# Performance work log

Measured on AMD Instinct MI355X. Metric: run time of the kernel, lower is better.

## Reference

```python
import jax, jax.numpy as jnp
import numpy as np

EPS_ENT = 1e-08


def setup_inputs() -> dict:
    key = jax.random.key(0)
    k1, k2, k3, k4 = jax.random.split(key, 4)
    B, K, D = 128, 64, 256      # batch, slots, d_model
    BD, NC = 2700, 1024          # basis_dim, num_codes
    slot_features = jax.random.normal(k1, (B, K, D), dtype=jnp.float32)
    W_proj = jax.random.normal(k2, (BD, D), dtype=jnp.float32) * (1.0 / np.sqrt(D))
    b_proj = jax.random.normal(k3, (BD,), dtype=jnp.float32) * 0.01
    embed = jax.random.normal(k4, (NC, BD), dtype=jnp.float32)
    return {"slot_features": slot_features, "W_proj": W_proj, "b_proj": b_proj, "embed": embed}


def reference(slot_features, W_proj, b_proj, embed):
    b, k, _ = slot_features.shape
    num_codes, basis_dim = embed.shape
    # slot_proj: Linear(d_model -> basis_dim)
    z_e = jnp.einsum('bkd,ed->bke', slot_features, W_proj) + b_proj  # [B,K,BD]
    z_flat = z_e.reshape(b * k, basis_dim)
    # squared-euclidean distances: ||z||^2 - 2 z e^T + ||e||^2  -> [B*K, NC]
    dist = (jnp.sum(z_flat * z_flat, axis=1, keepdims=True)
            - 2.0 * (z_flat @ embed.T)
            + jnp.sum(embed * embed, axis=1)[None, :])
    indices_flat = jnp.argmin(dist, axis=-1)                # [B*K]
    indices = indices_flat.reshape(b, k)
    e_i = embed[indices_flat].reshape(b, k, basis_dim)      # gather codebook atoms
    # straight-through estimator
    q_st = z_e + jax.lax.stop_gradient(e_i - z_e)
    vq_loss = jnp.mean((z_e - jax.lax.stop_gradient(e_i)) ** 2)
    # entropy diversity bonus over soft assignment distribution
    probs = jax.nn.softmax(-dist, axis=-1)                  # [B*K, NC]
    avg_probs = jnp.mean(probs, axis=0)
    entropy = -jnp.sum(avg_probs * jnp.log(avg_probs + EPS_ENT))
    return (q_st, indices, vq_loss, entropy)
```

## Files before the change

kernel.cpp:

```cpp
#include <hip/hip_runtime.h>
#include <stdint.h>
#include <stddef.h>

static constexpr int    M_ROWS = 8192;
static constexpr int    DMODEL = 256;
static constexpr int    BDIM   = 2700;
static constexpr int    NCODES = 1024;
static constexpr int    KP     = 2720;
static constexpr int    NPAD   = 2816;
static constexpr size_t QST_N  = (size_t)M_ROWS * (size_t)BDIM;
static constexpr int    MAX_CAND = 32768;

typedef __bf16 bf16x8 __attribute__((ext_vector_type(8)));
typedef float  f32x4  __attribute__((ext_vector_type(4)));

__device__ inline unsigned short bf16h(float x) {
    unsigned u = __float_as_uint(x);
    unsigned r = u + 0x7fffu + ((u >> 16) & 1u);
    return (unsigned short)(r >> 16);
}
__device__ inline float bf2f(unsigned short h) {
    return __uint_as_float(((unsigned)h) << 16);
}
__device__ inline void split3(float x, unsigned short& h, unsigned short& m,
                              unsigned short& l) {
    h = bf16h(x);
    const float r1 = x - bf2f(h);
    m = bf16h(r1);
    l = bf16h(r1 - bf2f(m));
}
__device__ inline unsigned long long pack_key(float v, int idx) {
    unsigned u = __float_as_uint(v);
    unsigned k = (u & 0x80000000u) ? ~u : (u | 0x80000000u);
    return ((unsigned long long)k << 32) | (unsigned)idx;
}
__device__ inline float unpack_val(unsigned long long key) {
    unsigned ku = (unsigned)(key >> 32);
    return (ku & 0x80000000u) ? __uint_as_float(ku & 0x7fffffffu)
                              : __uint_as_float(~ku);
}

__global__ __launch_bounds__(256)
void eprep(const float* __restrict__ emb, unsigned short* __restrict__ eh,
           float* __restrict__ esq, float* __restrict__ prob,
           float* __restrict__ sse, int* __restrict__ ccount,
           float* __restrict__ zsq)
{
    const int row = blockIdx.x;
    const int tid = threadIdx.x;
    if (tid < 8) zsq[row * 8 + tid] = 0.0f;
    if (tid == 0) prob[row] = 0.0f;
    if (row == 0 && tid == 0) { sse[0] = 0.0f; ccount[0] = 0; }

    float acc = 0.0f;
    for (int g = tid; g < KP / 4; g += 256) {
        const int c = g * 4;
        ushort4 h;
        if (c < BDIM) {
            const float4 v = *reinterpret_cast<const float4*>(emb + (size_t)row * BDIM + c);
            h.x = bf16h(v.x); h.y = bf16h(v.y); h.z = bf16h(v.z); h.w = bf16h(v.w);
            acc += v.x * v.x + v.y * v.y + v.z * v.z + v.w * v.w;
        } else {
            h.x = h.y = h.z = h.w = 0;
        }
        *reinterpret_cast<ushort4*>(eh + (size_t)row * KP + c) = h;
    }
    for (int off = 32; off; off >>= 1) acc += __shfl_down(acc, off);
    __shared__ float wsum[4];
    if ((tid & 63) == 0) wsum[tid >> 6] = acc;
    __syncthreads();
    if (tid == 0) esq[row] = wsum[0] + wsum[1] + wsum[2] + wsum[3];
}

__global__ __launch_bounds__(256)
void ssplit3(const float* __restrict__ slot, unsigned short* __restrict__ sh,
             unsigned short* __restrict__ sm, unsigned short* __restrict__ sl)
{
    const size_t i = (size_t)blockIdx.x * 256 + threadIdx.x;
    const float4 v = reinterpret_cast<const float4*>(slot)[i];
    ushort4 h, m, l;
    split3(v.x, h.x, m.x, l.x); split3(v.y, h.y, m.y, l.y);
    split3(v.z, h.z, m.z, l.z); split3(v.w, h.w, m.w, l.w);
    reinterpret_cast<ushort4*>(sh)[i] = h;
    reinterpret_cast<ushort4*>(sm)[i] = m;
    reinterpret_cast<ushort4*>(sl)[i] = l;
}

__global__ __launch_bounds__(64)
void wsplit3(const float* __restrict__ W, unsigned short* __restrict__ wh,
             unsigned short* __restrict__ wm, unsigned short* __restrict__ wl)
{
    const int row = blockIdx.x;
    const int c   = threadIdx.x * 4;
    ushort4 h, m, l;
    if (row < BDIM) {
        const float4 v = *reinterpret_cast<const float4*>(W + (size_t)row * DMODEL + c);
        split3(v.x, h.x, m.x, l.x); split3(v.y, h.y, m.y, l.y);
        split3(v.z, h.z, m.z, l.z); split3(v.w, h.w, m.w, l.w);
    } else {
        h.x = h.y = h.z = h.w = 0; m = h; l = h;
    }
    const size_t off = (size_t)row * DMODEL + c;
    *reinterpret_cast<ushort4*>(wh + off) = h;
    *reinterpret_cast<ushort4*>(wm + off) = m;
    *reinterpret_cast<ushort4*>(wl + off) = l;
}

__global__ __launch_bounds__(256, 2)
void gemm1_mfma(const unsigned short* __restrict__ Ah_, const unsigned short* __restrict__ Am_,
                const unsigned short* __restrict__ Al_,
                const unsigned short* __restrict__ Bh_, const unsigned short* __restrict__ Bm_,
                const unsigned short* __restrict__ Bl_,
                const float* __restrict__ bias, float* __restrict__ Z,
                unsigned short* __restrict__ zh, float* __restrict__ zsq)
{
    constexpr int NT = DMODEL / 32;
    __shared__ unsigned short lds[2][3 * 4096 + 3 * 2048];

    const int tid  = threadIdx.x;
    const int wid  = tid >> 6;
    const int lane = tid & 63;
    const int bid  = blockIdx.x;
    const int xcd  = bid & 7;
    const int q    = bid >> 3;
    const int row0 = (xcd * 8 + q / 44) << 7;
    const int col0 = (q % 44) << 6;
    const int wr = wid >> 1, wc = wid & 1;

    f32x4 acc[4][2];
#pragma unroll
    for (int m = 0; m < 4; ++m)
#pragma unroll
        for (int n = 0; n < 2; ++n) acc[m][n] = (f32x4)0.0f;

    auto stage = [&](int t, int b) {
        const int kt = t * 32;
#pragma unroll
        for (int T = 0; T < 3; ++T) {
            const unsigned short* src = (T == 0) ? Ah_ : (T == 1) ? Am_ : Al_;
#pragma unroll
            for (int qq = 0; qq < 2; ++qq) {
                const int chunk = wid * 2 + qq;
                const int r     = chunk * 16 + (lane >> 2);
                const int unswz = ((lane & 3) << 4) ^ ((r & 3) << 4);
                const unsigned short* g = src + (size_t)(row0 + r) * DMODEL + kt + (unswz >> 1);
                __builtin_amdgcn_global_load_lds(
                    (const __attribute__((address_space(1))) void*)g,
                    (__attribute__((address_space(3))) void*)(&lds[b][T * 4096 + chunk * 512]),
                    16, 0, 0);
            }
        }
#pragma unroll
        for (int T = 0; T < 3; ++T) {
            const unsigned short* src = (T == 0) ? Bh_ : (T == 1) ? Bm_ : Bl_;
            const int chunk = wid;
            const int r     = chunk * 16 + (lane >> 2);
            const int unswz = ((lane & 3) << 4) ^ ((r & 3) << 4);
            const unsigned short* g = src + (size_t)(col0 + r) * DMODEL + kt + (unswz >> 1);
            __builtin_amdgcn_global_load_lds(
                (const __attribute__((address_space(1))) void*)g,
                (__attribute__((address_space(3))) void*)(&lds[b][12288 + T * 2048 + chunk * 512]),
                16, 0, 0);
        }
    };

    auto compute = [&](int b) {
        bf16x8 ah[4], am[4], al[4], bh[2], bm[2], bl[2];
        const int kb = (lane >> 4) << 4;
#pragma unroll
        for (int m = 0; m < 4; ++m) {
            const int r   = wr * 64 + m * 16 + (lane & 15);
            const int off = r * 32 + ((kb ^ ((r & 3) << 4)) >> 1);
            ah[m] = *reinterpret_cast<const bf16x8*>(&lds[b][off]);
            am[m] = *reinterpret_cast<const bf16x8*>(&lds[b][4096 + off]);
            al[m] = *reinterpret_cast<const bf16x8*>(&lds[b][8192 + off]);
        }
#pragma unroll
        for (int n = 0; n < 2; ++n) {
            const int r   = wc * 32 + n * 16 + (lane & 15);
            const int off = r * 32 + ((kb ^ ((r & 3) << 4)) >> 1);
            bh[n] = *reinterpret_cast<const bf16x8*>(&lds[b][12288 + off]);
            bm[n] = *reinterpret_cast<const bf16x8*>(&lds[b][14336 + off]);
            bl[n] = *reinterpret_cast<const bf16x8*>(&lds[b][16384 + off]);
        }
#pragma unroll
        for (int m = 0; m < 4; ++m)
#pragma unroll
            for (int n = 0; n < 2; ++n) {
                acc[m][n] = __builtin_amdgcn_mfma_f32_16x16x32_bf16(ah[m], bh[n], acc[m][n], 0, 0, 0);
                acc[m][n] = __builtin_amdgcn_mfma_f32_16x16x32_bf16(ah[m], bm[n], acc[m][n], 0, 0, 0);
                acc[m][n] = __builtin_amdgcn_mfma_f32_16x16x32_bf16(am[m], bh[n], acc[m][n], 0, 0, 0);
                acc[m][n] = __builtin_amdgcn_mfma_f32_16x16x32_bf16(ah[m], bl[n], acc[m][n], 0, 0, 0);
                acc[m][n] = __builtin_amdgcn_mfma_f32_16x16x32_bf16(am[m], bm[n], acc[m][n], 0, 0, 0);
                acc[m][n] = __builtin_amdgcn_mfma_f32_16x16x32_bf16(al[m], bh[n], acc[m][n], 0, 0, 0);
            }
    };

    stage(0, 0);
    __syncthreads();
    for (int t = 0; t < NT; ++t) {
        const int cur = t & 1;
        if (t + 1 < NT) stage(t + 1, cur ^ 1);
        compute(cur);
        __syncthreads();
    }

    float bv[2];
    int   cv[2];
#pragma unroll
    for (int n = 0; n < 2; ++n) {
        cv[n] = col0 + wc * 32 + n * 16 + (lane & 15);
        bv[n] = (cv[n] < BDIM) ? bias[cv[n]] : 0.0f;
    }
#pragma unroll
    for (int m = 0; m < 4; ++m) {
        const int gr0 = row0 + wr * 64 + m * 16 + ((lane >> 4) << 2);
#pragma unroll
        for (int r = 0; r < 4; ++r) {
            const int gr = gr0 + r;
            float s2 = 0.0f;
#pragma unroll
            for (int n = 0; n < 2; ++n) {
                if (cv[n] < BDIM) {
                    const float z = acc[m][n][r] + bv[n];
                    Z[(size_t)gr * BDIM + cv[n]] = z;
                    zh[(size_t)gr * KP + cv[n]] = bf16h(z);
                    s2 = __builtin_fmaf(z, z, s2);
                } else if (cv[n] < KP) {
                    zh[(size_t)gr * KP + cv[n]] = 0;
                }
            }
            s2 += __shfl_xor(s2, 1);
            s2 += __shfl_xor(s2, 2);
            s2 += __shfl_xor(s2, 4);
            s2 += __shfl_xor(s2, 8);
            if ((lane & 15) == 0) atomicAdd(&zsq[gr], s2);
        }
    }
}

__global__ __launch_bounds__(256, 2)
void gemm2_mfma(const unsigned short* __restrict__ Ah, const unsigned short* __restrict__ Bh,
                const float* __restrict__ zsq, const float* __restrict__ esq,
                float* __restrict__ dist)
{
    constexpr int NT = KP / 32;
    __shared__ unsigned short lds[2][2][128 * 32];

    const int tid  = threadIdx.x;
    const int wid  = tid >> 6;
    const int lane = tid & 63;
    const int bid  = blockIdx.x;
    const int row0 = (bid >> 3) << 7;
    const int col0 = (bid & 7) << 7;
    const int wr = wid >> 1, wc = wid & 1;

    f32x4 acc[4][4];
#pragma unroll
    for (int m = 0; m < 4; ++m)
#pragma unroll
        for (int n = 0; n < 4; ++n) acc[m][n] = (f32x4)0.0f;

    auto stage = [&](int t, int b) {
        const int kt = t * 32;
#pragma unroll
        for (int T = 0; T < 2; ++T) {
            const int base = T ? col0 : row0;
            const unsigned short* src = T ? Bh : Ah;
#pragma unroll
            for (int q = 0; q < 2; ++q) {
                const int chunk = wid * 2 + q;
                const int r     = chunk * 16 + (lane >> 2);
                const int unswz = ((lane & 3) << 4) ^ ((r & 3) << 4);
                const unsigned short* g = src + (size_t)(base + r) * KP + kt + (unswz >> 1);
                __builtin_amdgcn_global_load_lds(
                    (const __attribute__((address_space(1))) void*)g,
                    (__attribute__((address_space(3))) void*)(&lds[b][T][chunk * 512]),
                    16, 0, 0);
            }
        }
    };

    auto compute = [&](int b) {
        bf16x8 ah[4], bh[4];
        const int kb = (lane >> 4) << 4;
#pragma unroll
        for (int m = 0; m < 4; ++m) {
            const int r   = wr * 64 + m * 16 + (lane & 15);
            const int off = r * 32 + ((kb ^ ((r & 3) << 4)) >> 1);
            ah[m] = *reinterpret_cast<const bf16x8*>(&lds[b][0][off]);
        }
#pragma unroll
        for (int n = 0; n < 4; ++n) {
            const int r   = wc * 64 + n * 16 + (lane & 15);
            const int off = r * 32 + ((kb ^ ((r & 3) << 4)) >> 1);
            bh[n] = *reinterpret_cast<const bf16x8*>(&lds[b][1][off]);
        }
#pragma unroll
        for (int m = 0; m < 4; ++m)
#pragma unroll
            for (int n = 0; n < 4; ++n)
                acc[m][n] = __builtin_amdgcn_mfma_f32_16x16x32_bf16(ah[m], bh[n], acc[m][n], 0, 0, 0);
    };

    stage(0, 0);
    __syncthreads();
    for (int t = 0; t < NT; ++t) {
        const int cur = t & 1;
        if (t + 1 < NT) stage(t + 1, cur ^ 1);
        compute(cur);
        __syncthreads();
    }

#pragma unroll
    for (int m = 0; m < 4; ++m) {
        const int gr0 = row0 + wr * 64 + m * 16 + ((lane >> 4) << 2);
#pragma unroll
        for (int n = 0; n < 4; ++n) {
            const int gc = col0 + wc * 64 + n * 16 + (lane & 15);
            const float eq = esq[gc];
#pragma unroll
            for (int r = 0; r < 4; ++r) {
                const int gr = gr0 + r;
                dist[(size_t)gr * NCODES + gc] = zsq[gr] - 2.0f * acc[m][n][r] + eq;
            }
        }
    }
}

static constexpr float DELTA = 3.0f;

__global__ __launch_bounds__(256)
void row_softmax32(const float* __restrict__ dist, float* __restrict__ prob_acc,
                   float* __restrict__ sse, float* __restrict__ out_idx_f,
                   int* __restrict__ out_idx_i, float* __restrict__ gap_out,
                   unsigned* __restrict__ cand, int* __restrict__ cand_count,
                   unsigned long long* __restrict__ row_best)
{
    const int tid = threadIdx.x;
    __shared__ unsigned long long wm0[4], wm1[4];
    __shared__ float wred[4];
    float pacc[4] = {0.f, 0.f, 0.f, 0.f};
    float sse_loc = 0.f;

    for (int rr = 0; rr < 32; ++rr) {
        const int row = blockIdx.x * 32 + rr;
        const float4 d4 = reinterpret_cast<const float4*>(dist + (size_t)row * NCODES)[tid];
        const float dv[4] = {d4.x, d4.y, d4.z, d4.w};

        unsigned long long b0 = 0xFFFFFFFFFFFFFFFFull, b1 = 0xFFFFFFFFFFFFFFFFull;
#pragma unroll
        for (int j = 0; j < 4; ++j) {
            const unsigned long long k = pack_key(dv[j], tid * 4 + j);
            if (k < b0) { b1 = b0; b0 = k; } else if (k < b1) { b1 = k; }
        }
        for (int off = 1; off < 64; off <<= 1) {
            const unsigned long long o0 = __shfl_xor(b0, off);
            const unsigned long long o1 = __shfl_xor(b1, off);
            const unsigned long long nb0 = (b0 < o0) ? b0 : o0;
            const unsigned long long mx  = (b0 < o0) ? o0 : b0;
            const unsigned long long mn1 = (b1 < o1) ? b1 : o1;
            b0 = nb0;
            b1 = (mx < mn1) ? mx : mn1;
        }
        __syncthreads();
        if ((tid & 63) == 0) { wm0[tid >> 6] = b0; wm1[tid >> 6] = b1; }
        __syncthreads();
        unsigned long long B0 = wm0[0], B1 = wm1[0];
#pragma unroll
        for (int w = 1; w < 4; ++w) {
            const unsigned long long o0 = wm0[w], o1 = wm1[w];
            const unsigned long long nb0 = (B0 < o0) ? B0 : o0;
            const unsigned long long mx  = (B0 < o0) ? o0 : B0;
            const unsigned long long mn1 = (B1 < o1) ? B1 : o1;
            B0 = nb0;
            B1 = (mx < mn1) ? mx : mn1;
        }
        const float m   = unpack_val(B0);
        const int   idx = (int)(B0 & 0xffffffffu);
        const float gap = unpack_val(B1) - m;

        if (gap < DELTA) {
            if (tid == 0) row_best[row] = 0xFFFFFFFFFFFFFFFFull;
#pragma unroll
            for (int j = 0; j < 4; ++j) {
                if (dv[j] - m < DELTA) {
                    const int slot = atomicAdd(cand_count, 1);
                    if (slot < MAX_CAND)
                        cand[slot] = ((unsigned)row << 10) | (unsigned)(tid * 4 + j);
                }
            }
        }

        float e[4];
        float s_local = 0.0f;
#pragma unroll
        for (int j = 0; j < 4; ++j) { e[j] = expf(m - dv[j]); s_local += e[j]; }
        for (int off = 32; off; off >>= 1) s_local += __shfl_down(s_local, off);
        if ((tid & 63) == 0) wred[tid >> 6] = s_local;
        __syncthreads();
        const float S = wred[0] + wred[1] + wred[2] + wred[3];
        const float inv = 1.0f / S;
#pragma unroll
        for (int j = 0; j < 4; ++j) pacc[j] += e[j] * inv;

        if (tid == 0) {
            out_idx_f[row] = (float)idx;
            out_idx_i[row] = idx;
            gap_out[row]   = gap;
            sse_loc += m;
        }
    }

    const float scale = 0.0001220703125f;
#pragma unroll
    for (int j = 0; j < 4; ++j)
        if (pacc[j] > 0.0f) atomicAdd(&prob_acc[tid * 4 + j], pacc[j] * scale);
    if (tid == 0) atomicAdd(sse, sse_loc);
}

__global__ __launch_bounds__(256)
void refine2(const float* __restrict__ Zf, const float* __restrict__ emb,
             const unsigned* __restrict__ cand, const int* __restrict__ cand_count,
             const float* __restrict__ zsq, const float* __restrict__ esq,
             unsigned long long* __restrict__ row_best)
{
    const int nwaves = gridDim.x * 4;
    const int wglob  = blockIdx.x * 4 + (threadIdx.x >> 6);
    const int lane   = threadIdx.x & 63;
    const int n = min(*cand_count, MAX_CAND);
    for (int e = wglob; e < n; e += nwaves) {
        const unsigned pc  = cand[e];
        const int row  = (int)(pc >> 10);
        const int code = (int)(pc & 1023u);
        const float4* zp = reinterpret_cast<const float4*>(Zf + (size_t)row * BDIM);
        const float4* ep = reinterpret_cast<const float4*>(emb + (size_t)code * BDIM);
        float a0 = 0, a1 = 0, a2 = 0, a3 = 0;
        for (int k = lane; k < BDIM / 4; k += 64) {
            const float4 z4 = zp[k];
            const float4 e4 = ep[k];
            a0 = __builtin_fmaf(z4.x, e4.x, a0);
            a1 = __builtin_fmaf(z4.y, e4.y, a1);
            a2 = __builtin_fmaf(z4.z, e4.z, a2);
            a3 = __builtin_fmaf(z4.w, e4.w, a3);
        }
        float t = (a0 + a1) + (a2 + a3);
        for (int off = 32; off; off >>= 1) t += __shfl_down(t, off);
        if (lane == 0) {
            const float d = zsq[row] - 2.0f * t + esq[code];
            atomicMin(&row_best[row], pack_key(d, code));
        }
    }
}

__global__ __launch_bounds__(256)
void gather_fix(const float* __restrict__ embed, const float* __restrict__ gap,
                const unsigned long long* __restrict__ row_best,
                int* __restrict__ idxi, float* __restrict__ idxf,
                float* __restrict__ q)
{
    const int row = blockIdx.x;
    __shared__ int code_s;
    if (threadIdx.x == 0) {
        int code = idxi[row];
        if (gap[row] < DELTA) {
            const unsigned long long k = row_best[row];
            if (k != 0xFFFFFFFFFFFFFFFFull) {
                code = (int)(k & 0xffffffffu);
                idxi[row] = code;
                idxf[row] = (float)code;
            }
        }
        code_s = code;
    }
    __syncthreads();
    const int code = code_s;
    const float4* s = reinterpret_cast<const float4*>(embed + (size_t)code * BDIM);
    float4*       d = reinterpret_cast<float4*>(q + (size_t)row * BDIM);
    for (int i = threadIdx.x; i < (BDIM >> 2); i += 256) d[i] = s[i];
}

__global__ __launch_bounds__(256)
void finalize(const float* __restrict__ prob_acc, const float* __restrict__ sse,
              float* __restrict__ out)
{
    const int tid = threadIdx.x;
    float ent = 0.0f;
    for (int c = tid; c < NCODES; c += 256) {
        const float a = prob_acc[c];
        ent -= a * logf(a + 1e-8f);
    }
    for (int off = 32; off; off >>= 1) ent += __shfl_down(ent, off);
    __shared__ float wred[4];
    if ((tid & 63) == 0) wred[tid >> 6] = ent;
    __syncthreads();
    if (tid == 0) {
        out[QST_N + M_ROWS + 0] = sse[0] / 22118400.0f;
        out[QST_N + M_ROWS + 1] = wred[0] + wred[1] + wred[2] + wred[3];
    }
}

extern "C" void kernel_launch(void* const* d_in, const int* in_sizes, int n_in,
                              void* d_out, int out_size, void* d_ws, size_t ws_size,
                              hipStream_t stream)
{
    (void)in_sizes; (void)n_in; (void)out_size; (void)ws_size;
    const float* slot = (const float*)d_in[0];
    const float* W    = (const float*)d_in[1];
    const float* bpr  = (const float*)d_in[2];
    const float* emb  = (const float*)d_in[3];

    float* out  = (float*)d_out;
    float* Z    = out;
    float* idxf = out + QST_N;

    const size_t DIST_B = (size_t)M_ROWS * NCODES * 4;
    const size_t ZH_B   = (size_t)M_ROWS * KP * 2;
    const size_t EH_B   = (size_t)NCODES * KP * 2;

    char* w = (char*)d_ws;
    float* dist = (float*)w;                          w += DIST_B;
    const size_t SSPL_B = (size_t)M_ROWS * DMODEL * 2;
    const size_t WSPL_B = (size_t)NPAD   * DMODEL * 2;
    unsigned short* sh3 = (unsigned short*)(char*)dist;
    unsigned short* sm3 = (unsigned short*)((char*)dist + SSPL_B);
    unsigned short* sl3 = (unsigned short*)((char*)dist + 2 * SSPL_B);
    unsigned short* wh3 = (unsigned short*)((char*)dist + 3 * SSPL_B);
    unsigned short* wm3 = (unsigned short*)((char*)dist + 3 * SSPL_B + WSPL_B);
    unsigned short* wl3 = (unsigned short*)((char*)dist + 3 * SSPL_B + 2 * WSPL_B);

    unsigned short* zh = (unsigned short*)w;          w += ZH_B;
    unsigned short* eh = (unsigned short*)w;          w += EH_B;
    float* zsq  = (float*)w;                          w += (size_t)M_ROWS * 4;
    float* esq  = (float*)w;                          w += (size_t)NCODES * 4;
    float* gap  = (float*)w;                          w += (size_t)M_ROWS * 4;
    int*   idxi = (int*)w;                            w += (size_t)M_ROWS * 4;
    float* prob = (float*)w;                          w += (size_t)NCODES * 4;
    float* sse  = (float*)w;                          w += 256;
    unsigned long long* rbest = (unsigned long long*)w; w += (size_t)M_ROWS * 8;
    unsigned* cand = (unsigned*)w;                    w += (size_t)MAX_CAND * 4;
    int* ccount = (int*)w;

    eprep<<<NCODES, 256, 0, stream>>>(emb, eh, esq, prob, sse, ccount, zsq);
    ssplit3<<<(M_ROWS * DMODEL / 4) / 256, 256, 0, stream>>>(slot, sh3, sm3, sl3);
    wsplit3<<<NPAD, 64, 0, stream>>>(W, wh3, wm3, wl3);
    gemm1_mfma<<<(NPAD / 64) * (M_ROWS / 128), 256, 0, stream>>>(
        sh3, sm3, sl3, wh3, wm3, wl3, bpr, Z, zh, zsq);
    gemm2_mfma<<<(NCODES / 128) * (M_ROWS / 128), 256, 0, stream>>>(
        zh, eh, zsq, esq, dist);
    row_softmax32<<<M_ROWS / 32, 256, 0, stream>>>(dist, prob, sse, idxf, idxi, gap,
                                                   cand, ccount, rbest);
    refine2<<<256, 256, 0, stream>>>(Z, emb, cand, ccount, zsq, esq, rbest);
    gather_fix<<<M_ROWS, 256, 0, stream>>>(emb, gap, rbest, idxi, idxf, Z);
    finalize<<<1, 256, 0, stream>>>(prob, sse, out);
}
```

Before: 409.0 us.

## Use bf16x2 split for projection GEMM and merge prep kernels

```diff
diff --git a/kernel.cpp b/kernel.cpp
--- a/kernel.cpp
+++ b/kernel.cpp
@@ -22,12 +22,9 @@
 __device__ inline float bf2f(unsigned short h) {
     return __uint_as_float(((unsigned)h) << 16);
 }
-__device__ inline void split3(float x, unsigned short& h, unsigned short& m,
-                              unsigned short& l) {
+__device__ inline void split2(float x, unsigned short& h, unsigned short& l) {
     h = bf16h(x);
-    const float r1 = x - bf2f(h);
-    m = bf16h(r1);
-    l = bf16h(r1 - bf2f(m));
+    l = bf16h(x - bf2f(h));
 }
 __device__ inline unsigned long long pack_key(float v, int idx) {
     unsigned u = __float_as_uint(v);
@@ -41,81 +38,72 @@
 }
 
 __global__ __launch_bounds__(256)
-void eprep(const float* __restrict__ emb, unsigned short* __restrict__ eh,
-           float* __restrict__ esq, float* __restrict__ prob,
-           float* __restrict__ sse, int* __restrict__ ccount,
-           float* __restrict__ zsq)
-{
-    const int row = blockIdx.x;
+void prep(const float* __restrict__ emb, const float* __restrict__ W,
+          const float* __restrict__ slot,
+          unsigned short* __restrict__ eh, float* __restrict__ esq,
+          unsigned short* __restrict__ wh2, unsigned short* __restrict__ wm2,
+          unsigned short* __restrict__ sh2, unsigned short* __restrict__ sl2,
+          float* __restrict__ prob, float* __restrict__ sse,
+          int* __restrict__ ccount, float* __restrict__ zsq)
+{
+    const int bid = blockIdx.x;
     const int tid = threadIdx.x;
-    if (tid < 8) zsq[row * 8 + tid] = 0.0f;
-    if (tid == 0) prob[row] = 0.0f;
-    if (row == 0 && tid == 0) { sse[0] = 0.0f; ccount[0] = 0; }
-
-    float acc = 0.0f;
-    for (int g = tid; g < KP / 4; g += 256) {
-        const int c = g * 4;
-        ushort4 h;
-        if (c < BDIM) {
-            const float4 v = *reinterpret_cast<const float4*>(emb + (size_t)row * BDIM + c);
-            h.x = bf16h(v.x); h.y = bf16h(v.y); h.z = bf16h(v.z); h.w = bf16h(v.w);
-            acc += v.x * v.x + v.y * v.y + v.z * v.z + v.w * v.w;
+    if (bid < NCODES) {
+        const int row = bid;
+        if (tid < 8) zsq[row * 8 + tid] = 0.0f;
+        if (tid == 0) prob[row] = 0.0f;
+        if (row == 0 && tid == 0) { sse[0] = 0.0f; ccount[0] = 0; }
+        float acc = 0.0f;
+        for (int g = tid; g < KP / 4; g += 256) {
+            const int c = g * 4;
+            ushort4 h;
+            if (c < BDIM) {
+                const float4 v = *reinterpret_cast<const float4*>(emb + (size_t)row * BDIM + c);
+                h.x = bf16h(v.x); h.y = bf16h(v.y); h.z = bf16h(v.z); h.w = bf16h(v.w);
+                acc += v.x * v.x + v.y * v.y + v.z * v.z + v.w * v.w;
+            } else {
+                h.x = h.y = h.z = h.w = 0;
+            }
+            *reinterpret_cast<ushort4*>(eh + (size_t)row * KP + c) = h;
+        }
+        for (int off = 32; off; off >>= 1) acc += __shfl_down(acc, off);
+        __shared__ float wsum[4];
+        if ((tid & 63) == 0) wsum[tid >> 6] = acc;
+        __syncthreads();
+        if (tid == 0) esq[row] = wsum[0] + wsum[1] + wsum[2] + wsum[3];
+    } else if (bid < NCODES + NPAD / 4) {
+        const int row = (bid - NCODES) * 4 + (tid >> 6);
+        const int c   = (tid & 63) * 4;
+        ushort4 h, m;
+        if (row < BDIM) {
+            const float4 v = *reinterpret_cast<const float4*>(W + (size_t)row * DMODEL + c);
+            split2(v.x, h.x, m.x); split2(v.y, h.y, m.y);
+            split2(v.z, h.z, m.z); split2(v.w, h.w, m.w);
         } else {
-            h.x = h.y = h.z = h.w = 0;
-        }
-        *reinterpret_cast<ushort4*>(eh + (size_t)row * KP + c) = h;
-    }
-    for (int off = 32; off; off >>= 1) acc += __shfl_down(acc, off);
-    __shared__ float wsum[4];
-    if ((tid & 63) == 0) wsum[tid >> 6] = acc;
-    __syncthreads();
-    if (tid == 0) esq[row] = wsum[0] + wsum[1] + wsum[2] + wsum[3];
-}
-
-__global__ __launch_bounds__(256)
-void ssplit3(const float* __restrict__ slot, unsigned short* __restrict__ sh,
-             unsigned short* __restrict__ sm, unsigned short* __restrict__ sl)
-{
-    const size_t i = (size_t)blockIdx.x * 256 + threadIdx.x;
-    const float4 v = reinterpret_cast<const float4*>(slot)[i];
-    ushort4 h, m, l;
-    split3(v.x, h.x, m.x, l.x); split3(v.y, h.y, m.y, l.y);
-    split3(v.z, h.z, m.z, l.z); split3(v.w, h.w, m.w, l.w);
-    reinterpret_cast<ushort4*>(sh)[i] = h;
-    reinterpret_cast<ushort4*>(sm)[i] = m;
-    reinterpret_cast<ushort4*>(sl)[i] = l;
-}
-
-__global__ __launch_bounds__(64)
-void wsplit3(const float* __restrict__ W, unsigned short* __restrict__ wh,
-             unsigned short* __restrict__ wm, unsigned short* __restrict__ wl)
-{
-    const int row = blockIdx.x;
-    const int c   = threadIdx.x * 4;
-    ushort4 h, m, l;
-    if (row < BDIM) {
-        const float4 v = *reinterpret_cast<const float4*>(W + (size_t)row * DMODEL + c);
-        split3(v.x, h.x, m.x, l.x); split3(v.y, h.y, m.y, l.y);
-        split3(v.z, h.z, m.z, l.z); split3(v.w, h.w, m.w, l.w);
+            h.x = h.y = h.z = h.w = 0; m = h;
+        }
+        const size_t off = (size_t)row * DMODEL + c;
+        *reinterpret_cast<ushort4*>(wh2 + off) = h;
+        *reinterpret_cast<ushort4*>(wm2 + off) = m;
     } else {
-        h.x = h.y = h.z = h.w = 0; m = h; l = h;
-    }
-    const size_t off = (size_t)row * DMODEL + c;
-    *reinterpret_cast<ushort4*>(wh + off) = h;
-    *reinterpret_cast<ushort4*>(wm + off) = m;
-    *reinterpret_cast<ushort4*>(wl + off) = l;
-}
-
-__global__ __launch_bounds__(256, 2)
-void gemm1_mfma(const unsigned short* __restrict__ Ah_, const unsigned short* __restrict__ Am_,
-                const unsigned short* __restrict__ Al_,
+        const size_t i = (size_t)(bid - NCODES - NPAD / 4) * 256 + tid;
+        const float4 v = reinterpret_cast<const float4*>(slot)[i];
+        ushort4 h, l;
+        split2(v.x, h.x, l.x); split2(v.y, h.y, l.y);
+        split2(v.z, h.z, l.z); split2(v.w, h.w, l.w);
+        reinterpret_cast<ushort4*>(sh2)[i] = h;
+        reinterpret_cast<ushort4*>(sl2)[i] = l;
+    }
+}
+
+__global__ __launch_bounds__(256, 3)
+void gemm1_mfma(const unsigned short* __restrict__ Ah_, const unsigned short* __restrict__ Al_,
                 const unsigned short* __restrict__ Bh_, const unsigned short* __restrict__ Bm_,
-                const unsigned short* __restrict__ Bl_,
                 const float* __restrict__ bias, float* __restrict__ Z,
                 unsigned short* __restrict__ zh, float* __restrict__ zsq)
 {
     constexpr int NT = DMODEL / 32;
-    __shared__ unsigned short lds[2][3 * 4096 + 3 * 2048];
+    __shared__ unsigned short lds[2][2 * 4096 + 2 * 2048];
 
     const int tid  = threadIdx.x;
     const int wid  = tid >> 6;
@@ -136,13 +124,13 @@
     auto stage = [&](int t, int b) {
         const int kt = t * 32;
 #pragma unroll
-        for (int T = 0; T < 3; ++T) {
-            const unsigned short* src = (T == 0) ? Ah_ : (T == 1) ? Am_ : Al_;
+        for (int T = 0; T < 2; ++T) {
+            const unsigned short* src = T ? Al_ : Ah_;
 #pragma unroll
             for (int qq = 0; qq < 2; ++qq) {
                 const int chunk = wid * 2 + qq;
                 const int r     = chunk * 16 + (lane >> 2);
-                const int unswz = ((lane & 3) << 4) ^ ((r & 3) << 4);
+                const int unswz = ((lane & 3) << 4) ^ (((r >> 1) & 3) << 4);
                 const unsigned short* g = src + (size_t)(row0 + r) * DMODEL + kt + (unswz >> 1);
                 __builtin_amdgcn_global_load_lds(
                     (const __attribute__((address_space(1))) void*)g,
@@ -151,48 +139,44 @@
             }
         }
 #pragma unroll
-        for (int T = 0; T < 3; ++T) {
-            const unsigned short* src = (T == 0) ? Bh_ : (T == 1) ? Bm_ : Bl_;
+        for (int T = 0; T < 2; ++T) {
+            const unsigned short* src = T ? Bm_ : Bh_;
             const int chunk = wid;
             const int r     = chunk * 16 + (lane >> 2);
-            const int unswz = ((lane & 3) << 4) ^ ((r & 3) << 4);
+            const int unswz = ((lane & 3) << 4) ^ (((r >> 1) & 3) << 4);
             const unsigned short* g = src + (size_t)(col0 + r) * DMODEL + kt + (unswz >> 1);
             __builtin_amdgcn_global_load_lds(
                 (const __attribute__((address_space(1))) void*)g,
-                (__attribute__((address_space(3))) void*)(&lds[b][12288 + T * 2048 + chunk * 512]),
+                (__attribute__((address_space(3))) void*)(&lds[b][8192 + T * 2048 + chunk * 512]),
                 16, 0, 0);
         }
     };
 
     auto compute = [&](int b) {
-        bf16x8 ah[4], am[4], al[4], bh[2], bm[2], bl[2];
+        bf16x8 a0[4], a1[4], b0[2], b1[2];
         const int kb = (lane >> 4) << 4;
 #pragma unroll
         for (int m = 0; m < 4; ++m) {
             const int r   = wr * 64 + m * 16 + (lane & 15);
-            const int off = r * 32 + ((kb ^ ((r & 3) << 4)) >> 1);
-            ah[m] = *reinterpret_cast<const bf16x8*>(&lds[b][off]);
-            am[m] = *reinterpret_cast<const bf16x8*>(&lds[b][4096 + off]);
-            al[m] = *reinterpret_cast<const bf16x8*>(&lds[b][8192 + off]);
+            const int off = r * 32 + ((kb ^ (((r >> 1) & 3) << 4)) >> 1);
+            a0[m] = *reinterpret_cast<const bf16x8*>(&lds[b][off]);
+            a1[m] = *reinterpret_cast<const bf16x8*>(&lds[b][4096 + off]);
         }
 #pragma unroll
         for (int n = 0; n < 2; ++n) {
             const int r   = wc * 32 + n * 16 + (lane & 15);
-            const int off = r * 32 + ((kb ^ ((r & 3) << 4)) >> 1);
-            bh[n] = *reinterpret_cast<const bf16x8*>(&lds[b][12288 + off]);
-            bm[n] = *reinterpret_cast<const bf16x8*>(&lds[b][14336 + off]);
-            bl[n] = *reinterpret_cast<const bf16x8*>(&lds[b][16384 + off]);
+            const int off = r * 32 + ((kb ^ (((r >> 1) & 3) << 4)) >> 1);
+            b0[n] = *reinterpret_cast<const bf16x8*>(&lds[b][8192 + off]);
+            b1[n] = *reinterpret_cast<const bf16x8*>(&lds[b][10240 + off]);
         }
 #pragma unroll
         for (int m = 0; m < 4; ++m)
 #pragma unroll
             for (int n = 0; n < 2; ++n) {
-                acc[m][n] = __builtin_amdgcn_mfma_f32_16x16x32_bf16(ah[m], bh[n], acc[m][n], 0, 0, 0);
-                acc[m][n] = __builtin_amdgcn_mfma_f32_16x16x32_bf16(ah[m], bm[n], acc[m][n], 0, 0, 0);
-                acc[m][n] = __builtin_amdgcn_mfma_f32_16x16x32_bf16(am[m], bh[n], acc[m][n], 0, 0, 0);
-                acc[m][n] = __builtin_amdgcn_mfma_f32_16x16x32_bf16(ah[m], bl[n], acc[m][n], 0, 0, 0);
-                acc[m][n] = __builtin_amdgcn_mfma_f32_16x16x32_bf16(am[m], bm[n], acc[m][n], 0, 0, 0);
-                acc[m][n] = __builtin_amdgcn_mfma_f32_16x16x32_bf16(al[m], bh[n], acc[m][n], 0, 0, 0);
+                acc[m][n] = __builtin_amdgcn_mfma_f32_16x16x32_bf16(a0[m], b0[n], acc[m][n], 0, 0, 0);
+                acc[m][n] = __builtin_amdgcn_mfma_f32_16x16x32_bf16(a0[m], b1[n], acc[m][n], 0, 0, 0);
+                acc[m][n] = __builtin_amdgcn_mfma_f32_16x16x32_bf16(a1[m], b0[n], acc[m][n], 0, 0, 0);
+                acc[m][n] = __builtin_amdgcn_mfma_f32_16x16x32_bf16(a1[m], b1[n], acc[m][n], 0, 0, 0);
             }
     };
 
@@ -271,7 +255,7 @@
             for (int q = 0; q < 2; ++q) {
                 const int chunk = wid * 2 + q;
                 const int r     = chunk * 16 + (lane >> 2);
-                const int unswz = ((lane & 3) << 4) ^ ((r & 3) << 4);
+                const int unswz = ((lane & 3) << 4) ^ (((r >> 1) & 3) << 4);
                 const unsigned short* g = src + (size_t)(base + r) * KP + kt + (unswz >> 1);
                 __builtin_amdgcn_global_load_lds(
                     (const __attribute__((address_space(1))) void*)g,
@@ -287,13 +271,13 @@
 #pragma unroll
         for (int m = 0; m < 4; ++m) {
             const int r   = wr * 64 + m * 16 + (lane & 15);
-            const int off = r * 32 + ((kb ^ ((r & 3) << 4)) >> 1);
+            const int off = r * 32 + ((kb ^ (((r >> 1) & 3) << 4)) >> 1);
             ah[m] = *reinterpret_cast<const bf16x8*>(&lds[b][0][off]);
         }
 #pragma unroll
         for (int n = 0; n < 4; ++n) {
             const int r   = wc * 64 + n * 16 + (lane & 15);
-            const int off = r * 32 + ((kb ^ ((r & 3) << 4)) >> 1);
+            const int off = r * 32 + ((kb ^ (((r >> 1) & 3) << 4)) >> 1);
             bh[n] = *reinterpret_cast<const bf16x8*>(&lds[b][1][off]);
         }
 #pragma unroll
@@ -520,14 +504,10 @@
 
     char* w = (char*)d_ws;
     float* dist = (float*)w;                          w += DIST_B;
-    const size_t SSPL_B = (size_t)M_ROWS * DMODEL * 2;
-    const size_t WSPL_B = (size_t)NPAD   * DMODEL * 2;
-    unsigned short* sh3 = (unsigned short*)(char*)dist;
-    unsigned short* sm3 = (unsigned short*)((char*)dist + SSPL_B);
-    unsigned short* sl3 = (unsigned short*)((char*)dist + 2 * SSPL_B);
-    unsigned short* wh3 = (unsigned short*)((char*)dist + 3 * SSPL_B);
-    unsigned short* wm3 = (unsigned short*)((char*)dist + 3 * SSPL_B + WSPL_B);
-    unsigned short* wl3 = (unsigned short*)((char*)dist + 3 * SSPL_B + 2 * WSPL_B);
+    unsigned short* sh2 = (unsigned short*)dist;
+    unsigned short* sl2 = sh2 + (size_t)M_ROWS * DMODEL;
+    unsigned short* wh2 = sl2 + (size_t)M_ROWS * DMODEL;
+    unsigned short* wm2 = wh2 + (size_t)NPAD * DMODEL;
 
     unsigned short* zh = (unsigned short*)w;          w += ZH_B;
     unsigned short* eh = (unsigned short*)w;          w += EH_B;
@@ -541,11 +521,10 @@
     unsigned* cand = (unsigned*)w;                    w += (size_t)MAX_CAND * 4;
     int* ccount = (int*)w;
 
-    eprep<<<NCODES, 256, 0, stream>>>(emb, eh, esq, prob, sse, ccount, zsq);
-    ssplit3<<<(M_ROWS * DMODEL / 4) / 256, 256, 0, stream>>>(slot, sh3, sm3, sl3);
-    wsplit3<<<NPAD, 64, 0, stream>>>(W, wh3, wm3, wl3);
+    prep<<<NCODES + NPAD / 4 + (M_ROWS * DMODEL / 4) / 256, 256, 0, stream>>>(
+        emb, W, slot, eh, esq, wh2, wm2, sh2, sl2, prob, sse, ccount, zsq);
     gemm1_mfma<<<(NPAD / 64) * (M_ROWS / 128), 256, 0, stream>>>(
-        sh3, sm3, sl3, wh3, wm3, wl3, bpr, Z, zh, zsq);
+        sh2, sl2, wh2, wm2, bpr, Z, zh, zsq);
     gemm2_mfma<<<(NCODES / 128) * (M_ROWS / 128), 256, 0, stream>>>(
         zh, eh, zsq, esq, dist);
     row_softmax32<<<M_ROWS / 32, 256, 0, stream>>>(dist, prob, sse, idxf, idxi, gap,
```

Result: faster. 365.9 us (-10.5%).
